# Kernel optimization log

Hardware: AMD Instinct MI355X
Metric: run time of the kernel (lower is better)

The kernel has to match this reference:

```python
import jax, jax.numpy as jnp
import numpy as np

BINS = 256
MAXV = float(2 ** 14 - 1)
LAP_K = jnp.array([[0.0, 1.0, 0.0], [1.0, -4.0, 1.0], [0.0, 1.0, 0.0]], jnp.float32).reshape(1, 1, 3, 3)


def _soft_hist_entropy(flat):
    # flat: (B, N) in arbitrary range; per-image min-max normalize to [0,1]
    fmin = jnp.min(flat, axis=1, keepdims=True)
    fmax = jnp.max(flat, axis=1, keepdims=True)
    rng = fmax - fmin
    rng = jnp.where(rng == 0, jnp.ones_like(rng), rng)
    x = jnp.clip((flat - fmin) / rng, 0.0, 1.0)
    # Triangular soft-histogram weights clamp(1-|x-c_k|/bw, 0) are nonzero for at
    # most the 2 bins adjacent to x, so scatter-add instead of a (B,N,BINS) tensor.
    p = x * BINS - 0.5            # position in bin-center coordinates
    i0 = jnp.floor(p)
    w1 = p - i0                   # weight on bin i0+1
    w0 = 1.0 - w1                 # weight on bin i0
    i0i = i0.astype(jnp.int32)
    i1i = i0i + 1
    v0 = (i0i >= 0) & (i0i < BINS)
    v1 = (i1i >= 0) & (i1i < BINS)

    def hist_one(idx0, idx1, a0, a1, m0, m1):
        h = jnp.zeros((BINS,), flat.dtype)
        h = h.at[jnp.clip(idx0, 0, BINS - 1)].add(jnp.where(m0, a0, 0.0))
        h = h.at[jnp.clip(idx1, 0, BINS - 1)].add(jnp.where(m1, a1, 0.0))
        return h

    hist = jax.vmap(hist_one)(i0i, i1i, w0, w1, v0, v1)  # (B, BINS)
    hist = hist / (jnp.sum(hist, axis=1, keepdims=True) + 1e-10)
    ent = -jnp.sum(hist * jnp.log2(hist + 1e-10), axis=1)
    return ent / jnp.float32(np.log2(BINS))


def _extract_features(image):
    # normalize 14-bit input to [0,1] iff values exceed 1 (matches torch branch)
    image = jnp.where(jnp.max(image) > 1.0, image / MAXV, image)
    B = image.shape[0]
    flat = image.reshape(B, -1)
    variance = jnp.var(flat, axis=1, ddof=1)   # torch.var is unbiased
    mn = jnp.min(flat, axis=1)
    mx = jnp.max(flat, axis=1)
    ent = _soft_hist_entropy(flat)
    lap = jax.lax.conv_general_dilated(
        image, LAP_K, window_strides=(1, 1), padding=[(1, 1), (1, 1)],
        dimension_numbers=('NCHW', 'OIHW', 'NCHW'))
    lap_var = jnp.var(lap.reshape(B, -1), axis=1, ddof=1)
    return jnp.stack([variance, mn, mx, ent, lap_var], axis=1)  # (B, 5)


def setup_inputs() -> dict:
    key = jax.random.key(0)
    ks = jax.random.split(key, 4)
    image = jax.random.uniform(ks[0], (16, 1, 1024, 1280), jnp.float32) * MAXV
    # Kaiming normal fan_in (relu): std = sqrt(2 / fan_in); biases zero
    W1 = jax.random.normal(ks[1], (64, 5), jnp.float32) * np.float32(np.sqrt(2.0 / 5))
    W2 = jax.random.normal(ks[2], (64, 64), jnp.float32) * np.float32(np.sqrt(2.0 / 64))
    W3 = jax.random.normal(ks[3], (3, 64), jnp.float32) * np.float32(np.sqrt(2.0 / 64))
    return {
        'image': image,
        'W1': W1, 'b1': jnp.zeros((64,), jnp.float32),
        'W2': W2, 'b2': jnp.zeros((64,), jnp.float32),
        'W3': W3, 'b3': jnp.zeros((3,), jnp.float32),
    }


def reference(image, W1, b1, W2, b2, W3, b3):
    feats = _extract_features(image)                       # (B, 5)
    h = jax.nn.relu(feats @ W1.T + b1)
    h = jax.nn.relu(h @ W2.T + b2)
    logits = h @ W3.T + b3                                  # (B, 3)
    probs = jax.nn.softmax(logits, axis=1)
    class_ids = jnp.argmax(probs, axis=1)
    return class_ids, probs, feats
```

## Files before the change

kernel.cpp:

```cpp
#include <hip/hip_runtime.h>
#include <cfloat>
#include <math.h>

#define IMG_B 16
#define IMG_H 1024
#define IMG_W 1280
#define NPIX (IMG_H * IMG_W)
#define BINS 256
#define SLICES 64
#define NBLK (IMG_B * SLICES)
#define F4_PER_SLICE (16 * IMG_W / 4)

__device__ __forceinline__ unsigned encf(float f) {
    unsigned u = __float_as_uint(f);
    return (u >> 31) ? ~u : (u | 0x80000000u);
}
__device__ __forceinline__ float decf(unsigned u) {
    unsigned b = (u & 0x80000000u) ? (u & 0x7fffffffu) : ~u;
    return __uint_as_float(b);
}


__global__ __launch_bounds__(256) void k_pre(const float* __restrict__ img,
                                             uint2* __restrict__ mmp,
                                             double* __restrict__ mom) {
    const int blk = blockIdx.x;
    const int tid = threadIdx.x;
    const int b   = blk >> 6;
    const int sl  = blk & 63;
    const int lane = tid & 63, wv = tid >> 6;

    const float* base = img + (size_t)b * NPIX;
    const int r0 = sl * 16;

    float fs = 0.f, fs2 = 0.f, fls = 0.f, fls2 = 0.f;
    float fmn = FLT_MAX, fmx = -FLT_MAX;

    #pragma unroll 2
    for (int k = 0; k < 20; ++k) {
        int i   = tid + k * 256;
        int ri  = i / 320;
        int c   = i - ri * 320;
        int r   = r0 + ri;
        const float* rowf = base + (size_t)r * IMG_W;
        float4 m = ((const float4*)rowf)[c];
        float4 up = make_float4(0.f, 0.f, 0.f, 0.f);
        float4 dn = make_float4(0.f, 0.f, 0.f, 0.f);
        if (r > 0)          up = ((const float4*)(rowf - IMG_W))[c];
        if (r < IMG_H - 1)  dn = ((const float4*)(rowf + IMG_W))[c];
        float lft = (c > 0)   ? rowf[4 * c - 1] : 0.f;
        float rgt = (c < 319) ? rowf[4 * c + 4] : 0.f;

        fs  += (m.x + m.y) + (m.z + m.w);
        fs2 += (m.x * m.x + m.y * m.y) + (m.z * m.z + m.w * m.w);
        fmn = fminf(fmn, fminf(fminf(m.x, m.y), fminf(m.z, m.w)));
        fmx = fmaxf(fmx, fmaxf(fmaxf(m.x, m.y), fmaxf(m.z, m.w)));

        float l0 = up.x + dn.x + lft + m.y - 4.f * m.x;
        float l1 = up.y + dn.y + m.x + m.z - 4.f * m.y;
        float l2 = up.z + dn.z + m.y + m.w - 4.f * m.z;
        float l3 = up.w + dn.w + m.z + rgt - 4.f * m.w;
        fls  += (l0 + l1) + (l2 + l3);
        fls2 += (l0 * l0 + l1 * l1) + (l2 * l2 + l3 * l3);
    }

    for (int o = 32; o; o >>= 1) {
        fs   += __shfl_down(fs,   (unsigned)o, 64);
        fs2  += __shfl_down(fs2,  (unsigned)o, 64);
        fls  += __shfl_down(fls,  (unsigned)o, 64);
        fls2 += __shfl_down(fls2, (unsigned)o, 64);
        fmn = fminf(fmn, __shfl_down(fmn, (unsigned)o, 64));
        fmx = fmaxf(fmx, __shfl_down(fmx, (unsigned)o, 64));
    }
    __shared__ float swred[4][4];
    __shared__ float rmn[4], rmx[4];
    if (lane == 0) {
        swred[0][wv] = fs;  swred[1][wv] = fs2;
        swred[2][wv] = fls; swred[3][wv] = fls2;
        rmn[wv] = fmn; rmx[wv] = fmx;
    }
    __syncthreads();
    if (tid == 0) {
        double S   = (double)swred[0][0] + (double)swred[0][1] + (double)swred[0][2] + (double)swred[0][3];
        double S2  = (double)swred[1][0] + (double)swred[1][1] + (double)swred[1][2] + (double)swred[1][3];
        double LS  = (double)swred[2][0] + (double)swred[2][1] + (double)swred[2][2] + (double)swred[2][3];
        double LS2 = (double)swred[3][0] + (double)swred[3][1] + (double)swred[3][2] + (double)swred[3][3];
        mom[blk * 4 + 0] = S;  mom[blk * 4 + 1] = S2;
        mom[blk * 4 + 2] = LS; mom[blk * 4 + 3] = LS2;
        float mn = fminf(fminf(rmn[0], rmn[1]), fminf(rmn[2], rmn[3]));
        float mx = fmaxf(fmaxf(rmx[0], rmx[1]), fmaxf(rmx[2], rmx[3]));
        mmp[blk] = make_uint2(encf(mn), encf(mx));
    }
}

__global__ __launch_bounds__(256) void k_hist(const float* __restrict__ img,
                                              const uint2* __restrict__ mmp,
                                              unsigned* __restrict__ bhist) {
    const int blk = blockIdx.x;
    const int tid = threadIdx.x;
    const int b   = blk >> 6;

    __shared__ unsigned long long lh64[BINS + 1];
    __shared__ float sh_ab[2];

    if (tid < 64) {
        uint2 e = mmp[b * 64 + tid];
        unsigned emn = e.x, emx = e.y;
        for (int o = 32; o; o >>= 1) {
            emn = min(emn, (unsigned)__shfl_down(emn, (unsigned)o, 64));
            emx = max(emx, (unsigned)__shfl_down(emx, (unsigned)o, 64));
        }
        if (tid == 0) {
            float fmn = decf(emn), fmx = decf(emx);
            float rng = fmx - fmn;
            if (rng == 0.f) rng = 1.f;
            float a = 256.f / rng;
            float bb = -fmn * a - 0.5f;
            sh_ab[0] = a; sh_ab[1] = bb;
        }
    }
    lh64[tid] = 0ull;
    if (tid == 0) lh64[BINS] = 0ull;
    __syncthreads();

    const float a = sh_ab[0], bb = sh_ab[1];

    const float4* p = (const float4*)img + (size_t)blk * F4_PER_SLICE;
    #pragma unroll 2
    for (int k = 0; k < 20; ++k) {
        float4 v = p[tid + k * 256];
        #pragma unroll
        for (int j = 0; j < 4; ++j) {
            float vv = (j == 0) ? v.x : (j == 1) ? v.y : (j == 2) ? v.z : v.w;
            float pp = fminf(fmaxf(vv * a + bb, -0.5f), 255.5f);
            float fi = floorf(pp);
            int   i0 = (int)fi;
            unsigned w1q = (unsigned)((pp - fi) * 65536.f + 0.5f);
            atomicAdd(&lh64[i0 + 1], 0x100000000ull + (unsigned long long)w1q);
        }
    }
    __syncthreads();

    unsigned long long a0 = lh64[tid];
    unsigned long long a1 = lh64[tid + 1];
    unsigned long long h  = ((a1 >> 32) << 16) - (a1 & 0xffffffffull) + (a0 & 0xffffffffull);
    bhist[blk * BINS + tid] = (unsigned)h;
}

__global__ __launch_bounds__(256) void k_final(
    const unsigned* __restrict__ bhist, const double* __restrict__ mom,
    const uint2* __restrict__ mmp,
    const float* __restrict__ W1, const float* __restrict__ b1,
    const float* __restrict__ W2, const float* __restrict__ b2,
    const float* __restrict__ W3, const float* __restrict__ b3,
    float* __restrict__ out)
{
    const int ib = blockIdx.x;
    const int tid = threadIdx.x;
    const int lane = tid & 63, wv = tid >> 6;

    __shared__ double dred[4];
    __shared__ float  fred[4];
    __shared__ double smom[4];
    __shared__ unsigned smm2[2];
    __shared__ unsigned sgm[4];
    __shared__ float f5[5], h1[64], h2[64], lg[3];

    double h = 0.0;
    for (int s = 0; s < 64; ++s)
        h += (double)bhist[(ib * 64 + s) * BINS + tid];

    double tot = h;
    for (int o = 32; o; o >>= 1) tot += __shfl_down(tot, (unsigned)o, 64);
    if (lane == 0) dred[wv] = tot;
    __syncthreads();
    tot = dred[0] + dred[1] + dred[2] + dred[3];

    double hv = h * (1.0 / 65536.0);
    double tv = tot * (1.0 / 65536.0);
    float hn = (float)(hv / (tv + 1e-10));
    float ce = hn * log2f(hn + 1e-10f);
    for (int o = 32; o; o >>= 1) ce += __shfl_down(ce, (unsigned)o, 64);
    if (lane == 0) fred[wv] = ce;

    if (tid < 64) {
        double q0 = mom[(ib * 64 + tid) * 4 + 0];
        double q1 = mom[(ib * 64 + tid) * 4 + 1];
        double q2 = mom[(ib * 64 + tid) * 4 + 2];
        double q3 = mom[(ib * 64 + tid) * 4 + 3];
        uint2 e = mmp[ib * 64 + tid];
        unsigned emn = e.x, emx = e.y;
        for (int o = 32; o; o >>= 1) {
            q0 += __shfl_down(q0, (unsigned)o, 64);
            q1 += __shfl_down(q1, (unsigned)o, 64);
            q2 += __shfl_down(q2, (unsigned)o, 64);
            q3 += __shfl_down(q3, (unsigned)o, 64);
            emn = min(emn, (unsigned)__shfl_down(emn, (unsigned)o, 64));
            emx = max(emx, (unsigned)__shfl_down(emx, (unsigned)o, 64));
        }
        if (tid == 0) {
            smom[0] = q0; smom[1] = q1; smom[2] = q2; smom[3] = q3;
            smm2[0] = emn; smm2[1] = emx;
        }
    }
    {
        unsigned g = max(max(mmp[tid].y, mmp[256 + tid].y),
                         max(mmp[512 + tid].y, mmp[768 + tid].y));
        for (int o = 32; o; o >>= 1)
            g = max(g, (unsigned)__shfl_down(g, (unsigned)o, 64));
        if (lane == 0) sgm[wv] = g;
    }
    __syncthreads();

    if (tid == 0) {
        float ent = -(fred[0] + fred[1] + fred[2] + fred[3]) / 8.f;
        float gmax = decf(max(max(sgm[0], sgm[1]), max(sgm[2], sgm[3])));
        float sc = (gmax > 1.f) ? (1.f / 16383.f) : 1.f;
        double N = (double)NPIX;
        double S = smom[0], S2 = smom[1], LS = smom[2], LS2 = smom[3];
        double sc2 = (double)sc * (double)sc;
        float var  = (float)((S2  - S  * S  / N) / (N - 1.0) * sc2);
        float lvar = (float)((LS2 - LS * LS / N) / (N - 1.0) * sc2);
        float mn = decf(smm2[0]) * sc;
        float mx = decf(smm2[1]) * sc;
        float* fo = out + 64 + ib * 5;
        fo[0] = var; fo[1] = mn; fo[2] = mx; fo[3] = ent; fo[4] = lvar;
        f5[0] = var; f5[1] = mn; f5[2] = mx; f5[3] = ent; f5[4] = lvar;
    }
    __syncthreads();

    if (tid < 64) {
        float aa = b1[tid];
        #pragma unroll
        for (int k = 0; k < 5; ++k) aa += W1[tid * 5 + k] * f5[k];
        h1[tid] = fmaxf(aa, 0.f);
    }
    __syncthreads();
    if (tid < 64) {
        float a2 = b2[tid];
        #pragma unroll
        for (int k = 0; k < 64; ++k) a2 += W2[tid * 64 + k] * h1[k];
        h2[tid] = fmaxf(a2, 0.f);
    }
    __syncthreads();
    if (tid < 3) {
        float a3 = b3[tid];
        #pragma unroll
        for (int k = 0; k < 64; ++k) a3 += W3[tid * 64 + k] * h2[k];
        lg[tid] = a3;
    }
    __syncthreads();
    if (tid == 0) {
        float m = fmaxf(lg[0], fmaxf(lg[1], lg[2]));
        float e0 = expf(lg[0] - m), e1 = expf(lg[1] - m), e2 = expf(lg[2] - m);
        float inv = 1.f / (e0 + e1 + e2);
        float p0 = e0 * inv, p1 = e1 * inv, p2 = e2 * inv;
        out[16 + ib * 3 + 0] = p0;
        out[16 + ib * 3 + 1] = p1;
        out[16 + ib * 3 + 2] = p2;
        int cid = 0; float bm = p0;
        if (p1 > bm) { bm = p1; cid = 1; }
        if (p2 > bm) { bm = p2; cid = 2; }
        out[ib] = (float)cid;
    }
}

extern "C" void kernel_launch(void* const* d_in, const int* in_sizes, int n_in,
                              void* d_out, int out_size, void* d_ws, size_t ws_size,
                              hipStream_t stream) {
    const float* img = (const float*)d_in[0];
    const float* W1  = (const float*)d_in[1];
    const float* b1  = (const float*)d_in[2];
    const float* W2  = (const float*)d_in[3];
    const float* b2  = (const float*)d_in[4];
    const float* W3  = (const float*)d_in[5];
    const float* b3  = (const float*)d_in[6];
    float* out = (float*)d_out;

    char* ws = (char*)d_ws;
    uint2*    mmp   = (uint2*)ws;
    double*   mom   = (double*)(ws + 8192);
    unsigned* bhist = (unsigned*)(ws + 40960);

    k_pre  <<<NBLK, 256, 0, stream>>>(img, mmp, mom);
    k_hist <<<NBLK, 256, 0, stream>>>(img, mmp, bhist);
    k_final<<<IMG_B, 256, 0, stream>>>(bhist, mom, mmp,
                                       W1, b1, W2, b2, W3, b3, out);
}
```

Measured before the change: 157.7 us.

## Fuse histogram and final MLP via global atomics and last-block completion

Merges the histogram kernel and the final per-image kernel into one launch. Each slice block atomically adds its partial histogram into a per-image 64-bit global histogram, and a counter picks the last-finishing block to compute entropy, features and the MLP. This removes one kernel launch and the 64-way partial-histogram readback, at the cost of global atomics and a tail where one block per image does the final work. Zeroing of the accumulators moves into the pre-pass kernel.

```diff
diff --git a/kernel.cpp b/kernel.cpp
--- a/kernel.cpp
+++ b/kernel.cpp
@@ -23,12 +23,19 @@
 
 __global__ __launch_bounds__(256) void k_pre(const float* __restrict__ img,
                                              uint2* __restrict__ mmp,
-                                             double* __restrict__ mom) {
+                                             double* __restrict__ mom,
+                                             unsigned long long* __restrict__ imgHist,
+                                             unsigned* __restrict__ cnt) {
     const int blk = blockIdx.x;
     const int tid = threadIdx.x;
     const int b   = blk >> 6;
     const int sl  = blk & 63;
     const int lane = tid & 63, wv = tid >> 6;
+
+    if (blk < IMG_B) {
+        imgHist[blk * BINS + tid] = 0ull;
+        if (tid == 0) cnt[blk] = 0u;
+    }
 
     const float* base = img + (size_t)b * NPIX;
     const int r0 = sl * 16;
@@ -93,15 +100,23 @@
     }
 }
 
-__global__ __launch_bounds__(256) void k_hist(const float* __restrict__ img,
-                                              const uint2* __restrict__ mmp,
-                                              unsigned* __restrict__ bhist) {
+__global__ __launch_bounds__(256) void k_fused(
+    const float* __restrict__ img, const uint2* __restrict__ mmp,
+    const double* __restrict__ mom,
+    unsigned long long* __restrict__ imgHist, unsigned* __restrict__ cnt,
+    const float* __restrict__ W1, const float* __restrict__ b1,
+    const float* __restrict__ W2, const float* __restrict__ b2,
+    const float* __restrict__ W3, const float* __restrict__ b3,
+    float* __restrict__ out)
+{
     const int blk = blockIdx.x;
     const int tid = threadIdx.x;
     const int b   = blk >> 6;
+    const int lane = tid & 63, wv = tid >> 6;
 
     __shared__ unsigned long long lh64[BINS + 1];
     __shared__ float sh_ab[2];
+    __shared__ unsigned slast;
 
     if (tid < 64) {
         uint2 e = mmp[b * 64 + tid];
@@ -141,23 +156,20 @@
     }
     __syncthreads();
 
-    unsigned long long a0 = lh64[tid];
-    unsigned long long a1 = lh64[tid + 1];
-    unsigned long long h  = ((a1 >> 32) << 16) - (a1 & 0xffffffffull) + (a0 & 0xffffffffull);
-    bhist[blk * BINS + tid] = (unsigned)h;
-}
-
-__global__ __launch_bounds__(256) void k_final(
-    const unsigned* __restrict__ bhist, const double* __restrict__ mom,
-    const uint2* __restrict__ mmp,
-    const float* __restrict__ W1, const float* __restrict__ b1,
-    const float* __restrict__ W2, const float* __restrict__ b2,
-    const float* __restrict__ W3, const float* __restrict__ b3,
-    float* __restrict__ out)
-{
-    const int ib = blockIdx.x;
-    const int tid = threadIdx.x;
-    const int lane = tid & 63, wv = tid >> 6;
+    {
+        unsigned long long a0 = lh64[tid];
+        unsigned long long a1 = lh64[tid + 1];
+        unsigned long long h  = ((a1 >> 32) << 16) - (a1 & 0xffffffffull) + (a0 & 0xffffffffull);
+        atomicAdd(&imgHist[b * BINS + tid], h);
+    }
+    __threadfence();
+    __syncthreads();
+    if (tid == 0) slast = (atomicAdd(&cnt[b], 1u) == 63u) ? 1u : 0u;
+    __syncthreads();
+    if (!slast) return;
+    __threadfence();
+
+    const int ib = b;
 
     __shared__ double dred[4];
     __shared__ float  fred[4];
@@ -166,9 +178,7 @@
     __shared__ unsigned sgm[4];
     __shared__ float f5[5], h1[64], h2[64], lg[3];
 
-    double h = 0.0;
-    for (int s = 0; s < 64; ++s)
-        h += (double)bhist[(ib * 64 + s) * BINS + tid];
+    double h = (double)imgHist[ib * BINS + tid];
 
     double tot = h;
     for (int o = 32; o; o >>= 1) tot += __shfl_down(tot, (unsigned)o, 64);
@@ -278,12 +288,12 @@
     float* out = (float*)d_out;
 
     char* ws = (char*)d_ws;
-    uint2*    mmp   = (uint2*)ws;
-    double*   mom   = (double*)(ws + 8192);
-    unsigned* bhist = (unsigned*)(ws + 40960);
-
-    k_pre  <<<NBLK, 256, 0, stream>>>(img, mmp, mom);
-    k_hist <<<NBLK, 256, 0, stream>>>(img, mmp, bhist);
-    k_final<<<IMG_B, 256, 0, stream>>>(bhist, mom, mmp,
-                                       W1, b1, W2, b2, W3, b3, out);
-}
+    uint2*              mmp     = (uint2*)ws;
+    double*             mom     = (double*)(ws + 8192);
+    unsigned long long* imgHist = (unsigned long long*)(ws + 40960);
+    unsigned*           cnt     = (unsigned*)(ws + 73728);
+
+    k_pre  <<<NBLK, 256, 0, stream>>>(img, mmp, mom, imgHist, cnt);
+    k_fused<<<NBLK, 256, 0, stream>>>(img, mmp, mom, imgHist, cnt,
+                                      W1, b1, W2, b2, W3, b3, out);
+}
```

After: 234.5 us. 1.49x slower.
